# Performance work log

Hardware: AMD Instinct MI355X
Metric: run time of the kernel (lower is better)

Reference implementation:

```python
import jax, jax.numpy as jnp
import numpy as np

D_MODEL, D_STATE, B, S = 1024, 64, 8, 2048


def setup_inputs() -> dict:
    key = jax.random.key(0)
    ks = jax.random.split(key, 14)
    inp = {"x": jax.random.normal(ks[0], (B, S, D_MODEL), jnp.float32)}
    names = ["cog", "beh", "env", "delta", "Bp", "Cp"]
    for i, n in enumerate(names):
        inp[f"W_{n}"] = jax.random.normal(ks[1 + 2 * i], (D_STATE, D_MODEL), jnp.float32) / np.sqrt(D_MODEL)
        inp[f"b_{n}"] = jnp.zeros((D_STATE,), jnp.float32)
    # torch init is log(|randn|+1e-4); we use strictly-negative A_log so the
    # length-2048 multiplicative recurrence stays finite (A_log is a learned
    # parameter, so its value is free; the math of forward is unchanged).
    inp["A_log"] = -jnp.abs(jax.random.normal(ks[13], (D_STATE, D_STATE), jnp.float32)) - 0.1
    return inp


def reference(x, W_cog, b_cog, W_beh, b_beh, W_env, b_env,
              W_delta, b_delta, W_Bp, b_Bp, W_Cp, b_Cp, A_log):
    # gating terms (computed in the source but never used downstream)
    A_t = (jax.nn.sigmoid(x @ W_cog.T + b_cog)
           * jax.nn.sigmoid(x @ W_beh.T + b_beh)
           * jax.nn.sigmoid(x @ W_env.T + b_env))
    del A_t

    delta = jax.nn.softplus(x @ W_delta.T + b_delta)   # [B,S,N]
    Bt = x @ W_Bp.T + b_Bp                             # [B,S,N]
    Ct = x @ W_Cp.T + b_Cp                             # [B,S,N]
    u = Bt * x[:, :, :D_STATE]                         # [B,S,N]

    # Faithful to torch broadcasting: after step 0 the carried state h is
    # [B,N,N] with h[b,i,j] = exp(A_log[i,j]*delta[b,t,i]) * h_prev[b,i,j] + u[b,t,j]
    def step(h, td):
        d, u_t, c_t = td                               # each [B,N]
        A = jnp.exp(A_log[None, :, :] * d[:, :, None]) # [B,N,N]
        h = A * h + u_t[:, None, :]
        y = jnp.einsum('bj,bij->bi', c_t, h)           # [B,N]
        return h, y

    h0 = jnp.zeros((x.shape[0], D_STATE, D_STATE), x.dtype)
    _, ys = jax.lax.scan(
        step, h0,
        (delta.transpose(1, 0, 2), u.transpose(1, 0, 2), Ct.transpose(1, 0, 2)))
    # torch stacks y_t of shape [B,1,N] along dim=1 -> [B,S,1,N]
    return ys.transpose(1, 0, 2)[:, :, None, :]
```

## Files before the change

### kernel.cpp

```cpp
#include <hip/hip_runtime.h>
#include <math.h>

#define DM   1024
#define DS   64
#define BATCH 8
#define SEQ  2048
#define CL   32
#define NC   64

typedef __bf16 bf16x8 __attribute__((ext_vector_type(8)));
typedef __bf16 bf16x4 __attribute__((ext_vector_type(4)));
typedef float  f32x4  __attribute__((ext_vector_type(4)));

__global__ __launch_bounds__(256) void wconv_kernel(
    const float* __restrict__ Wd, const float* __restrict__ Wb,
    const float* __restrict__ Wc, __bf16* __restrict__ Wp)
{
    int idx = blockIdx.x * 256 + threadIdx.x;
    int k  = idx & 1023;
    int n  = idx >> 10;
    const float* W = (n < 64) ? Wd : (n < 128 ? Wb : Wc);
    float v = W[(size_t)(n & 63) * DM + k];
    int kt = k >> 5, kk = k & 31;
    Wp[((size_t)kt * 192 + n) * 32 + kk] = (__bf16)v;
}

__global__ __launch_bounds__(256) void proj_mfma(
    const float* __restrict__ x, const __bf16* __restrict__ Wp,
    const float* __restrict__ bd, const float* __restrict__ bb,
    const float* __restrict__ bc,
    float* __restrict__ delta_g, float* __restrict__ u_g,
    float* __restrict__ ct_g)
{
    __shared__ __bf16 sA[2][32 * 40];
    __shared__ __bf16 sB[2][192 * 40];

    const int tid  = threadIdx.x;
    const int row0 = blockIdx.x * 32;

    const int sx_row = tid >> 3;
    const int sx_sub = tid & 7;
    const float* xg = x + (size_t)(row0 + sx_row) * DM + sx_sub * 4;
    const int wn0  = tid >> 2;
    const int wsub = tid & 3;

    const int lane = tid & 63, wv = tid >> 6;
    const int l15 = lane & 15, quad = lane >> 4;
    const int mrow  = (wv & 1) * 16;
    const int nbase = (wv >> 1) * 96;

    f32x4 acc[6];
    #pragma unroll
    for (int i = 0; i < 6; ++i) acc[i] = (f32x4){0.f, 0.f, 0.f, 0.f};

    float4 xr;
    uint4 w0, w1, w2;

    #define LOAD(kt) do {                                                     \
        xr = *(const float4*)(xg + (kt) * 32);                                \
        const __bf16* wp = Wp + ((size_t)(kt) * 192) * 32 + wsub * 8;         \
        w0 = *(const uint4*)(wp + (size_t)(wn0      ) * 32);                  \
        w1 = *(const uint4*)(wp + (size_t)(wn0 +  64) * 32);                  \
        w2 = *(const uint4*)(wp + (size_t)(wn0 + 128) * 32);                  \
    } while (0)

    #define STAGE(bi) do {                                                    \
        bf16x4 hv = {(__bf16)xr.x, (__bf16)xr.y, (__bf16)xr.z, (__bf16)xr.w}; \
        *(bf16x4*)&sA[bi][sx_row * 40 + sx_sub * 4] = hv;                     \
        *(uint4*)&sB[bi][(wn0      ) * 40 + wsub * 8] = w0;                   \
        *(uint4*)&sB[bi][(wn0 +  64) * 40 + wsub * 8] = w1;                   \
        *(uint4*)&sB[bi][(wn0 + 128) * 40 + wsub * 8] = w2;                   \
    } while (0)

    #define COMPUTE(bi) do {                                                  \
        bf16x8 ah = *(const bf16x8*)&sA[bi][(mrow + l15) * 40 + quad * 8];    \
        _Pragma("unroll")                                                     \
        for (int nt = 0; nt < 6; ++nt) {                                      \
            bf16x8 bf = *(const bf16x8*)                                      \
                &sB[bi][(nbase + nt * 16 + l15) * 40 + quad * 8];             \
            acc[nt] = __builtin_amdgcn_mfma_f32_16x16x32_bf16(                \
                ah, bf, acc[nt], 0, 0, 0);                                    \
        }                                                                     \
    } while (0)

    LOAD(0);
    STAGE(0);
    __syncthreads();

    int buf = 0;
    for (int kt = 0; kt < 32; ++kt) {
        if (kt < 31) LOAD(kt + 1);
        COMPUTE(buf);
        if (kt < 31) STAGE(buf ^ 1);
        __syncthreads();
        buf ^= 1;
    }

    #pragma unroll
    for (int nt = 0; nt < 6; ++nt) {
        int gn  = nbase + nt * 16 + l15;
        int mat = gn >> 6;
        int col = gn & 63;
        float bias = (mat == 0) ? bd[col] : (mat == 1 ? bb[col] : bc[col]);
        #pragma unroll
        for (int r = 0; r < 4; ++r) {
            int m = row0 + mrow + quad * 4 + r;
            float v = acc[nt][r] + bias;
            if (mat == 0) {
                float sp = (v > 20.f) ? v : log1pf(__expf(v));
                delta_g[(size_t)m * DS + col] = sp;
            } else if (mat == 1) {
                u_g[(size_t)m * DS + col] = v * x[(size_t)m * DM + col];
            } else {
                ct_g[(size_t)m * DS + col] = v;
            }
        }
    }
    #undef LOAD
    #undef STAGE
    #undef COMPUTE
}

__global__ __launch_bounds__(256) void pass1_kernel(
    const float* __restrict__ delta_g, const float* __restrict__ u_g,
    const float* __restrict__ A_log,
    float* __restrict__ E, float* __restrict__ Dsum)
{
    __shared__ float s_d[CL * 64];
    __shared__ float s_u[CL * 64];
    const int c = blockIdx.x, b = blockIdx.y, tid = threadIdx.x;
    const int t0 = c * CL;

    const float4* dg = (const float4*)(delta_g + ((size_t)b * SEQ + t0) * DS);
    const float4* ug = (const float4*)(u_g     + ((size_t)b * SEQ + t0) * DS);
    #pragma unroll
    for (int it = 0; it < (CL * 64 / 4) / 256; ++it) {
        int f = tid + it * 256;
        ((float4*)s_d)[f] = dg[f];
        ((float4*)s_u)[f] = ug[f];
    }

    const int i  = tid & 63;
    const int jg = tid >> 6;
    float alog[16];
    {
        const float4* ar = (const float4*)(A_log + i * 64 + jg * 16);
        #pragma unroll
        for (int q = 0; q < 4; ++q) {
            float4 v = ar[q];
            alog[4*q+0] = v.x; alog[4*q+1] = v.y;
            alog[4*q+2] = v.z; alog[4*q+3] = v.w;
        }
    }
    __syncthreads();

    float h[16];
    #pragma unroll
    for (int k = 0; k < 16; ++k) h[k] = 0.f;
    float dsum = 0.f;

    for (int t = 0; t < CL; ++t) {
        float d = s_d[t * 64 + i];
        dsum += d;
        const float* up = s_u + t * 64 + jg * 16;
        #pragma unroll
        for (int k = 0; k < 16; ++k)
            h[k] = __expf(alog[k] * d) * h[k] + up[k];
    }

    float* eo = E + (((size_t)c * BATCH + b) * 64 + i) * 64 + jg * 16;
    #pragma unroll
    for (int q = 0; q < 4; ++q)
        ((float4*)eo)[q] = make_float4(h[4*q], h[4*q+1], h[4*q+2], h[4*q+3]);
    if (jg == 0) Dsum[((size_t)c * BATCH + b) * 64 + i] = dsum;
}

__global__ __launch_bounds__(256) void pass2_kernel(
    const float* __restrict__ A_log, const float* __restrict__ E,
    const float* __restrict__ Dsum, float* __restrict__ Sin)
{
    const int g = blockIdx.x * 256 + threadIdx.x;
    const int b = g >> 12;
    const int e = g & 4095;
    const int i = e >> 6;
    const float al = A_log[e];

    float Eb[4], db[4];
    #pragma unroll
    for (int p = 0; p < 4; ++p) {
        size_t nb = (size_t)p * BATCH + b;
        Eb[p] = E[nb * 4096 + e];
        db[p] = __expf(al * Dsum[nb * 64 + i]);
    }

    float carry = 0.f;
    #pragma unroll 4
    for (int c = 0; c < NC; ++c) {
        const int s = c & 3;
        float Ec = Eb[s], dc = db[s];
        if (c + 4 < NC) {
            size_t nb = (size_t)(c + 4) * BATCH + b;
            Eb[s] = E[nb * 4096 + e];
            db[s] = __expf(al * Dsum[nb * 64 + i]);
        }
        Sin[((size_t)c * BATCH + b) * 4096 + e] = carry;
        carry = dc * carry + Ec;
    }
}

__global__ __launch_bounds__(256) void pass3_kernel(
    const float* __restrict__ delta_g, const float* __restrict__ u_g,
    const float* __restrict__ ct_g, const float* __restrict__ A_log,
    const float* __restrict__ Sin, float* __restrict__ out)
{
    __shared__ float s_d[CL * 64];
    __shared__ float s_u[CL * 64];
    __shared__ float s_c[CL * 64];

    const int c = blockIdx.x, b = blockIdx.y, tid = threadIdx.x;
    const int t0 = c * CL;

    const float4* dg = (const float4*)(delta_g + ((size_t)b * SEQ + t0) * DS);
    const float4* ug = (const float4*)(u_g     + ((size_t)b * SEQ + t0) * DS);
    const float4* cg = (const float4*)(ct_g    + ((size_t)b * SEQ + t0) * DS);
    #pragma unroll
    for (int it = 0; it < (CL * 64 / 4) / 256; ++it) {
        int f = tid + it * 256;
        ((float4*)s_d)[f] = dg[f];
        ((float4*)s_u)[f] = ug[f];
        ((float4*)s_c)[f] = cg[f];
    }

    const int i  = tid >> 2;
    const int jg = tid & 3;

    float alog[16];
    {
        const float4* ar = (const float4*)(A_log + i * 64 + jg * 16);
        #pragma unroll
        for (int q = 0; q < 4; ++q) {
            float4 v = ar[q];
            alog[4*q+0] = v.x; alog[4*q+1] = v.y;
            alog[4*q+2] = v.z; alog[4*q+3] = v.w;
        }
    }

    float h[16];
    {
        const float4* hin = (const float4*)(
            Sin + (((size_t)c * BATCH + b) * 64 + i) * 64 + jg * 16);
        #pragma unroll
        for (int q = 0; q < 4; ++q) {
            float4 v = hin[q];
            h[4*q+0] = v.x; h[4*q+1] = v.y; h[4*q+2] = v.z; h[4*q+3] = v.w;
        }
    }
    __syncthreads();

    for (int t = 0; t < CL; ++t) {
        float d = s_d[t * 64 + i];
        const float* up = s_u + t * 64 + jg * 16;
        const float* cp = s_c + t * 64 + jg * 16;
        float part = 0.f;
        #pragma unroll
        for (int k = 0; k < 16; ++k) {
            h[k] = __expf(alog[k] * d) * h[k] + up[k];
            part += cp[k] * h[k];
        }
        part += __shfl_xor(part, 1);
        part += __shfl_xor(part, 2);
        if (jg == 0)
            out[((size_t)b * SEQ + t0 + t) * DS + i] = part;
    }
}

extern "C" void kernel_launch(void* const* d_in, const int* in_sizes, int n_in,
                              void* d_out, int out_size, void* d_ws, size_t ws_size,
                              hipStream_t stream)
{
    const float* x     = (const float*)d_in[0];
    const float* Wd    = (const float*)d_in[7];
    const float* bd    = (const float*)d_in[8];
    const float* Wb    = (const float*)d_in[9];
    const float* bb    = (const float*)d_in[10];
    const float* Wc    = (const float*)d_in[11];
    const float* bc    = (const float*)d_in[12];
    const float* A_log = (const float*)d_in[13];
    float* out = (float*)d_out;

    float* ws = (float*)d_ws;
    float* delta_g = ws;
    float* u_g     = ws + 1 * 1048576;
    float* ct_g    = ws + 2 * 1048576;
    float* E       = ws + 3 * 1048576;
    float* Sin     = ws + 5 * 1048576;
    float* Dsum    = ws + 7 * 1048576;
    __bf16* Wp     = (__bf16*)E;

    wconv_kernel<<<768, 256, 0, stream>>>(Wd, Wb, Wc, Wp);
    proj_mfma<<<512, 256, 0, stream>>>(
        x, Wp, bd, bb, bc, delta_g, u_g, ct_g);
    pass1_kernel<<<dim3(NC, BATCH), 256, 0, stream>>>(
        delta_g, u_g, A_log, E, Dsum);
    pass2_kernel<<<(BATCH * 4096) / 256, 256, 0, stream>>>(
        A_log, E, Dsum, Sin);
    pass3_kernel<<<dim3(NC, BATCH), 256, 0, stream>>>(
        delta_g, u_g, ct_g, A_log, Sin, out);
}
```

Baseline: 204.2 us.

## Restructure projection GEMM to register-direct split-K and use exp2 in scans

The projection kernel no longer stages x and weights through LDS. Each wave loads its A and B fragments straight from global memory into registers with double buffering, and K is split across wave pairs with an LDS reduction at the end. The scan kernels fold log2(e) into A_log so they can call exp2f directly instead of __expf. pass2 is relaunched with 64-thread blocks to get more blocks. The register-direct loads give up the weight reuse across waves that LDS provided and raise register pressure (24 uint4 buffers).

```diff
diff --git a/kernel.cpp b/kernel.cpp
--- a/kernel.cpp
+++ b/kernel.cpp
@@ -9,7 +9,6 @@
 #define NC   64
 
 typedef __bf16 bf16x8 __attribute__((ext_vector_type(8)));
-typedef __bf16 bf16x4 __attribute__((ext_vector_type(4)));
 typedef float  f32x4  __attribute__((ext_vector_type(4)));
 
 __global__ __launch_bounds__(256) void wconv_kernel(
@@ -32,93 +31,97 @@
     float* __restrict__ delta_g, float* __restrict__ u_g,
     float* __restrict__ ct_g)
 {
-    __shared__ __bf16 sA[2][32 * 40];
-    __shared__ __bf16 sB[2][192 * 40];
+    __shared__ float sAcc[2][64][48];
 
     const int tid  = threadIdx.x;
-    const int row0 = blockIdx.x * 32;
-
-    const int sx_row = tid >> 3;
-    const int sx_sub = tid & 7;
-    const float* xg = x + (size_t)(row0 + sx_row) * DM + sx_sub * 4;
-    const int wn0  = tid >> 2;
-    const int wsub = tid & 3;
-
-    const int lane = tid & 63, wv = tid >> 6;
-    const int l15 = lane & 15, quad = lane >> 4;
-    const int mrow  = (wv & 1) * 16;
-    const int nbase = (wv >> 1) * 96;
-
-    f32x4 acc[6];
-    #pragma unroll
-    for (int i = 0; i < 6; ++i) acc[i] = (f32x4){0.f, 0.f, 0.f, 0.f};
-
-    float4 xr;
-    uint4 w0, w1, w2;
-
-    #define LOAD(kt) do {                                                     \
-        xr = *(const float4*)(xg + (kt) * 32);                                \
-        const __bf16* wp = Wp + ((size_t)(kt) * 192) * 32 + wsub * 8;         \
-        w0 = *(const uint4*)(wp + (size_t)(wn0      ) * 32);                  \
-        w1 = *(const uint4*)(wp + (size_t)(wn0 +  64) * 32);                  \
-        w2 = *(const uint4*)(wp + (size_t)(wn0 + 128) * 32);                  \
+    const int wv   = tid >> 6;
+    const int lane = tid & 63;
+    const int l15  = lane & 15, quad = lane >> 4;
+    const int w_m  = wv & 1;
+    const int w_k  = wv >> 1;
+    const int row0 = blockIdx.x * 32 + w_m * 16;
+
+    const float*  xg = x + (size_t)(row0 + l15) * DM + quad * 8;
+    const __bf16* wg = Wp + (size_t)l15 * 32 + quad * 8;
+
+    f32x4 acc[12];
+    #pragma unroll
+    for (int i = 0; i < 12; ++i) acc[i] = (f32x4){0.f, 0.f, 0.f, 0.f};
+
+    float4 aA0, aA1, aB0, aB1;
+    uint4  bA[12], bB[12];
+
+    #define LOADA(s0, s1, kt) do {                                            \
+        s0 = *(const float4*)(xg + (kt) * 32);                                \
+        s1 = *(const float4*)(xg + (kt) * 32 + 4);                            \
     } while (0)
-
-    #define STAGE(bi) do {                                                    \
-        bf16x4 hv = {(__bf16)xr.x, (__bf16)xr.y, (__bf16)xr.z, (__bf16)xr.w}; \
-        *(bf16x4*)&sA[bi][sx_row * 40 + sx_sub * 4] = hv;                     \
-        *(uint4*)&sB[bi][(wn0      ) * 40 + wsub * 8] = w0;                   \
-        *(uint4*)&sB[bi][(wn0 +  64) * 40 + wsub * 8] = w1;                   \
-        *(uint4*)&sB[bi][(wn0 + 128) * 40 + wsub * 8] = w2;                   \
+    #define LOADB(dst, kt) do {                                               \
+        const __bf16* p = wg + (size_t)(kt) * (192 * 32);                     \
+        _Pragma("unroll")                                                     \
+        for (int nt = 0; nt < 12; ++nt)                                       \
+            dst[nt] = *(const uint4*)(p + (size_t)nt * (16 * 32));            \
     } while (0)
-
-    #define COMPUTE(bi) do {                                                  \
-        bf16x8 ah = *(const bf16x8*)&sA[bi][(mrow + l15) * 40 + quad * 8];    \
+    #define COMPUTE(s0, s1, bsrc) do {                                        \
+        bf16x8 av = {(__bf16)s0.x, (__bf16)s0.y, (__bf16)s0.z, (__bf16)s0.w,  \
+                     (__bf16)s1.x, (__bf16)s1.y, (__bf16)s1.z, (__bf16)s1.w}; \
         _Pragma("unroll")                                                     \
-        for (int nt = 0; nt < 6; ++nt) {                                      \
-            bf16x8 bf = *(const bf16x8*)                                      \
-                &sB[bi][(nbase + nt * 16 + l15) * 40 + quad * 8];             \
+        for (int nt = 0; nt < 12; ++nt)                                       \
             acc[nt] = __builtin_amdgcn_mfma_f32_16x16x32_bf16(                \
-                ah, bf, acc[nt], 0, 0, 0);                                    \
-        }                                                                     \
+                av, __builtin_bit_cast(bf16x8, bsrc[nt]), acc[nt], 0, 0, 0);  \
     } while (0)
 
-    LOAD(0);
-    STAGE(0);
+    const int kt0 = w_k * 16;
+    LOADA(aA0, aA1, kt0);
+    LOADB(bA, kt0);
+
+    #pragma unroll
+    for (int k2 = 0; k2 < 8; ++k2) {
+        const int kt = kt0 + k2 * 2;
+        LOADB(bB, kt + 1);
+        LOADA(aB0, aB1, kt + 1);
+        COMPUTE(aA0, aA1, bA);
+        if (k2 < 7) {
+            LOADA(aA0, aA1, kt + 2);
+            LOADB(bA, kt + 2);
+        }
+        COMPUTE(aB0, aB1, bB);
+    }
+    #undef LOADA
+    #undef LOADB
+    #undef COMPUTE
+
+    if (w_k == 1) {
+        #pragma unroll
+        for (int nt = 0; nt < 12; ++nt)
+            *(f32x4*)&sAcc[w_m][lane][nt * 4] = acc[nt];
+    }
     __syncthreads();
-
-    int buf = 0;
-    for (int kt = 0; kt < 32; ++kt) {
-        if (kt < 31) LOAD(kt + 1);
-        COMPUTE(buf);
-        if (kt < 31) STAGE(buf ^ 1);
-        __syncthreads();
-        buf ^= 1;
-    }
-
-    #pragma unroll
-    for (int nt = 0; nt < 6; ++nt) {
-        int gn  = nbase + nt * 16 + l15;
-        int mat = gn >> 6;
-        int col = gn & 63;
-        float bias = (mat == 0) ? bd[col] : (mat == 1 ? bb[col] : bc[col]);
-        #pragma unroll
-        for (int r = 0; r < 4; ++r) {
-            int m = row0 + mrow + quad * 4 + r;
-            float v = acc[nt][r] + bias;
-            if (mat == 0) {
-                float sp = (v > 20.f) ? v : log1pf(__expf(v));
-                delta_g[(size_t)m * DS + col] = sp;
-            } else if (mat == 1) {
-                u_g[(size_t)m * DS + col] = v * x[(size_t)m * DM + col];
-            } else {
-                ct_g[(size_t)m * DS + col] = v;
+    if (w_k == 0) {
+        #pragma unroll
+        for (int nt = 0; nt < 12; ++nt) {
+            f32x4 o = *(const f32x4*)&sAcc[w_m][lane][nt * 4];
+            acc[nt] += o;
+        }
+        #pragma unroll
+        for (int nt = 0; nt < 12; ++nt) {
+            int mat = nt >> 2;
+            int col = ((nt & 3) << 4) + l15;
+            float bias = (mat == 0) ? bd[col] : (mat == 1 ? bb[col] : bc[col]);
+            #pragma unroll
+            for (int r = 0; r < 4; ++r) {
+                int m = row0 + quad * 4 + r;
+                float v = acc[nt][r] + bias;
+                if (mat == 0) {
+                    float sp = (v > 20.f) ? v : log1pf(__expf(v));
+                    delta_g[(size_t)m * DS + col] = sp;
+                } else if (mat == 1) {
+                    u_g[(size_t)m * DS + col] = v * x[(size_t)m * DM + col];
+                } else {
+                    ct_g[(size_t)m * DS + col] = v;
+                }
             }
         }
     }
-    #undef LOAD
-    #undef STAGE
-    #undef COMPUTE
 }
 
 __global__ __launch_bounds__(256) void pass1_kernel(
@@ -148,8 +151,8 @@
         #pragma unroll
         for (int q = 0; q < 4; ++q) {
             float4 v = ar[q];
-            alog[4*q+0] = v.x; alog[4*q+1] = v.y;
-            alog[4*q+2] = v.z; alog[4*q+3] = v.w;
+            alog[4*q+0] = v.x * 1.44269504f; alog[4*q+1] = v.y * 1.44269504f;
+            alog[4*q+2] = v.z * 1.44269504f; alog[4*q+3] = v.w * 1.44269504f;
         }
     }
     __syncthreads();
@@ -165,7 +168,7 @@
         const float* up = s_u + t * 64 + jg * 16;
         #pragma unroll
         for (int k = 0; k < 16; ++k)
-            h[k] = __expf(alog[k] * d) * h[k] + up[k];
+            h[k] = exp2f(alog[k] * d) * h[k] + up[k];
     }
 
     float* eo = E + (((size_t)c * BATCH + b) * 64 + i) * 64 + jg * 16;
@@ -175,22 +178,22 @@
     if (jg == 0) Dsum[((size_t)c * BATCH + b) * 64 + i] = dsum;
 }
 
-__global__ __launch_bounds__(256) void pass2_kernel(
+__global__ __launch_bounds__(64) void pass2_kernel(
     const float* __restrict__ A_log, const float* __restrict__ E,
     const float* __restrict__ Dsum, float* __restrict__ Sin)
 {
-    const int g = blockIdx.x * 256 + threadIdx.x;
+    const int g = blockIdx.x * 64 + threadIdx.x;
     const int b = g >> 12;
     const int e = g & 4095;
     const int i = e >> 6;
-    const float al = A_log[e];
+    const float al = A_log[e] * 1.44269504f;
 
     float Eb[4], db[4];
     #pragma unroll
     for (int p = 0; p < 4; ++p) {
         size_t nb = (size_t)p * BATCH + b;
         Eb[p] = E[nb * 4096 + e];
-        db[p] = __expf(al * Dsum[nb * 64 + i]);
+        db[p] = exp2f(al * Dsum[nb * 64 + i]);
     }
 
     float carry = 0.f;
@@ -201,7 +204,7 @@
         if (c + 4 < NC) {
             size_t nb = (size_t)(c + 4) * BATCH + b;
             Eb[s] = E[nb * 4096 + e];
-            db[s] = __expf(al * Dsum[nb * 64 + i]);
+            db[s] = exp2f(al * Dsum[nb * 64 + i]);
         }
         Sin[((size_t)c * BATCH + b) * 4096 + e] = carry;
         carry = dc * carry + Ec;
@@ -240,8 +243,8 @@
         #pragma unroll
         for (int q = 0; q < 4; ++q) {
             float4 v = ar[q];
-            alog[4*q+0] = v.x; alog[4*q+1] = v.y;
-            alog[4*q+2] = v.z; alog[4*q+3] = v.w;
+            alog[4*q+0] = v.x * 1.44269504f; alog[4*q+1] = v.y * 1.44269504f;
+            alog[4*q+2] = v.z * 1.44269504f; alog[4*q+3] = v.w * 1.44269504f;
         }
     }
 
@@ -264,7 +267,7 @@
         float part = 0.f;
         #pragma unroll
         for (int k = 0; k < 16; ++k) {
-            h[k] = __expf(alog[k] * d) * h[k] + up[k];
+            h[k] = exp2f(alog[k] * d) * h[k] + up[k];
             part += cp[k] * h[k];
         }
         part += __shfl_xor(part, 1);
@@ -302,7 +305,7 @@
         x, Wp, bd, bb, bc, delta_g, u_g, ct_g);
     pass1_kernel<<<dim3(NC, BATCH), 256, 0, stream>>>(
         delta_g, u_g, A_log, E, Dsum);
-    pass2_kernel<<<(BATCH * 4096) / 256, 256, 0, stream>>>(
+    pass2_kernel<<<512, 64, 0, stream>>>(
         A_log, E, Dsum, Sin);
     pass3_kernel<<<dim3(NC, BATCH), 256, 0, stream>>>(
         delta_g, u_g, ct_g, A_log, Sin, out);
```

After: 219.3 us. 7.4% more time.

## Retile projection GEMM with 32x32 MFMA, use exp2 in scan passes

Applied to the files above, without the earlier changes.

The projection GEMM now uses 64-row blocks with 32x32x16 bf16 MFMA instructions. It loads the x fragments straight from global memory into registers, dropping the A shared-memory staging, and double-buffers two K-tiles of weights per iteration. The scan kernels pre-scale A_log by log2(e) and use the hardware exp2 instruction instead of __expf. Pass2 prefetches eight chunks ahead instead of four. The aim is to cut LDS traffic, instruction count and the latency of exponentials, at the cost of more registers (launch bounds of 1 block) and fewer, larger GEMM blocks.

```diff
diff --git a/kernel.cpp b/kernel.cpp
--- a/kernel.cpp
+++ b/kernel.cpp
@@ -9,8 +9,14 @@
 #define NC   64
 
 typedef __bf16 bf16x8 __attribute__((ext_vector_type(8)));
-typedef __bf16 bf16x4 __attribute__((ext_vector_type(4)));
 typedef float  f32x4  __attribute__((ext_vector_type(4)));
+typedef float  f32x16 __attribute__((ext_vector_type(16)));
+
+#if __has_builtin(__builtin_amdgcn_exp2f)
+#define EXP2(v) __builtin_amdgcn_exp2f(v)
+#else
+#define EXP2(v) __expf(0.69314718056f * (v))
+#endif
 
 __global__ __launch_bounds__(256) void wconv_kernel(
     const float* __restrict__ Wd, const float* __restrict__ Wb,
@@ -25,89 +31,115 @@
     Wp[((size_t)kt * 192 + n) * 32 + kk] = (__bf16)v;
 }
 
-__global__ __launch_bounds__(256) void proj_mfma(
+__global__ __launch_bounds__(256, 1) void proj_mfma(
     const float* __restrict__ x, const __bf16* __restrict__ Wp,
     const float* __restrict__ bd, const float* __restrict__ bb,
     const float* __restrict__ bc,
     float* __restrict__ delta_g, float* __restrict__ u_g,
     float* __restrict__ ct_g)
 {
-    __shared__ __bf16 sA[2][32 * 40];
-    __shared__ __bf16 sB[2][192 * 40];
+    __shared__ __bf16 sB[2][192 * 72];
 
     const int tid  = threadIdx.x;
-    const int row0 = blockIdx.x * 32;
-
-    const int sx_row = tid >> 3;
-    const int sx_sub = tid & 7;
-    const float* xg = x + (size_t)(row0 + sx_row) * DM + sx_sub * 4;
-    const int wn0  = tid >> 2;
-    const int wsub = tid & 3;
+    const int row0 = blockIdx.x * 64;
 
     const int lane = tid & 63, wv = tid >> 6;
-    const int l15 = lane & 15, quad = lane >> 4;
-    const int mrow  = (wv & 1) * 16;
-    const int nbase = (wv >> 1) * 96;
-
-    f32x4 acc[6];
-    #pragma unroll
-    for (int i = 0; i < 6; ++i) acc[i] = (f32x4){0.f, 0.f, 0.f, 0.f};
-
-    float4 xr;
-    uint4 w0, w1, w2;
-
-    #define LOAD(kt) do {                                                     \
-        xr = *(const float4*)(xg + (kt) * 32);                                \
-        const __bf16* wp = Wp + ((size_t)(kt) * 192) * 32 + wsub * 8;         \
-        w0 = *(const uint4*)(wp + (size_t)(wn0      ) * 32);                  \
-        w1 = *(const uint4*)(wp + (size_t)(wn0 +  64) * 32);                  \
-        w2 = *(const uint4*)(wp + (size_t)(wn0 + 128) * 32);                  \
-    } while (0)
-
-    #define STAGE(bi) do {                                                    \
-        bf16x4 hv = {(__bf16)xr.x, (__bf16)xr.y, (__bf16)xr.z, (__bf16)xr.w}; \
-        *(bf16x4*)&sA[bi][sx_row * 40 + sx_sub * 4] = hv;                     \
-        *(uint4*)&sB[bi][(wn0      ) * 40 + wsub * 8] = w0;                   \
-        *(uint4*)&sB[bi][(wn0 +  64) * 40 + wsub * 8] = w1;                   \
-        *(uint4*)&sB[bi][(wn0 + 128) * 40 + wsub * 8] = w2;                   \
-    } while (0)
-
-    #define COMPUTE(bi) do {                                                  \
-        bf16x8 ah = *(const bf16x8*)&sA[bi][(mrow + l15) * 40 + quad * 8];    \
+    const int l31  = lane & 31, q = lane >> 5;
+    const int mbase = row0 + (wv & 1) * 32;
+    const int nhalf = (wv >> 1) * 96;
+
+    const float* xrow = x + (size_t)(mbase + l31) * DM;
+
+    f32x16 acc[3];
+    #pragma unroll
+    for (int i = 0; i < 3; ++i)
+        acc[i] = (f32x16){0,0,0,0,0,0,0,0,0,0,0,0,0,0,0,0};
+
+    float4 aC[8], aN[8];
+    uint4  wreg[6];
+
+    #define LOADB(kb) do {                                                    \
         _Pragma("unroll")                                                     \
-        for (int nt = 0; nt < 6; ++nt) {                                      \
-            bf16x8 bf = *(const bf16x8*)                                      \
-                &sB[bi][(nbase + nt * 16 + l15) * 40 + quad * 8];             \
-            acc[nt] = __builtin_amdgcn_mfma_f32_16x16x32_bf16(                \
-                ah, bf, acc[nt], 0, 0, 0);                                    \
+        for (int it = 0; it < 6; ++it) {                                      \
+            int g   = tid + it * 256;                                         \
+            int ktl = (it >= 3) ? 1 : 0;                                      \
+            int r   = g - ktl * 768;                                          \
+            int n   = r >> 2, c4 = r & 3;                                     \
+            wreg[it] = *(const uint4*)(                                       \
+                Wp + ((size_t)((kb) * 2 + ktl) * 192 + n) * 32 + c4 * 8);     \
         }                                                                     \
     } while (0)
-
-    LOAD(0);
-    STAGE(0);
+    #define STAGEB(bi) do {                                                   \
+        _Pragma("unroll")                                                     \
+        for (int it = 0; it < 6; ++it) {                                      \
+            int g   = tid + it * 256;                                         \
+            int ktl = (it >= 3) ? 1 : 0;                                      \
+            int r   = g - ktl * 768;                                          \
+            int n   = r >> 2, c4 = r & 3;                                     \
+            *(uint4*)&sB[bi][n * 72 + ktl * 32 + c4 * 8] = wreg[it];          \
+        }                                                                     \
+    } while (0)
+    #define LOADA(dst, kb) do {                                               \
+        _Pragma("unroll")                                                     \
+        for (int s = 0; s < 4; ++s) {                                         \
+            dst[2*s]   = *(const float4*)(xrow + (kb)*64 + s*16 + q*8);       \
+            dst[2*s+1] = *(const float4*)(xrow + (kb)*64 + s*16 + q*8 + 4);   \
+        }                                                                     \
+    } while (0)
+    #define COMPUTE(bi) do {                                                  \
+        _Pragma("unroll")                                                     \
+        for (int s = 0; s < 4; ++s) {                                         \
+            float4 a0 = aC[2*s], a1 = aC[2*s+1];                              \
+            bf16x8 av = {(__bf16)a0.x, (__bf16)a0.y, (__bf16)a0.z,            \
+                         (__bf16)a0.w, (__bf16)a1.x, (__bf16)a1.y,            \
+                         (__bf16)a1.z, (__bf16)a1.w};                         \
+            _Pragma("unroll")                                                 \
+            for (int nt = 0; nt < 3; ++nt) {                                  \
+                bf16x8 bv = *(const bf16x8*)                                  \
+                    &sB[bi][(nhalf + nt*32 + l31) * 72 + s*16 + q*8];         \
+                acc[nt] = __builtin_amdgcn_mfma_f32_32x32x16_bf16(            \
+                    av, bv, acc[nt], 0, 0, 0);                                \
+            }                                                                 \
+        }                                                                     \
+    } while (0)
+
+    LOADB(0);
+    STAGEB(0);
+    LOADA(aC, 0);
     __syncthreads();
 
     int buf = 0;
-    for (int kt = 0; kt < 32; ++kt) {
-        if (kt < 31) LOAD(kt + 1);
+    for (int kb = 0; kb < 16; ++kb) {
+        if (kb < 15) {
+            LOADB(kb + 1);
+            LOADA(aN, kb + 1);
+        }
         COMPUTE(buf);
-        if (kt < 31) STAGE(buf ^ 1);
+        if (kb < 15) STAGEB(buf ^ 1);
         __syncthreads();
+        if (kb < 15) {
+            #pragma unroll
+            for (int i = 0; i < 8; ++i) aC[i] = aN[i];
+        }
         buf ^= 1;
     }
-
-    #pragma unroll
-    for (int nt = 0; nt < 6; ++nt) {
-        int gn  = nbase + nt * 16 + l15;
-        int mat = gn >> 6;
+    #undef LOADB
+    #undef STAGEB
+    #undef LOADA
+    #undef COMPUTE
+
+    #pragma unroll
+    for (int nt = 0; nt < 3; ++nt) {
+        int gn  = nhalf + nt * 32 + l31;
+        int mat = (nhalf + nt * 32) >> 6;
         int col = gn & 63;
         float bias = (mat == 0) ? bd[col] : (mat == 1 ? bb[col] : bc[col]);
         #pragma unroll
-        for (int r = 0; r < 4; ++r) {
-            int m = row0 + mrow + quad * 4 + r;
+        for (int r = 0; r < 16; ++r) {
+            int m = mbase + (r & 3) + 8 * (r >> 2) + 4 * q;
             float v = acc[nt][r] + bias;
             if (mat == 0) {
-                float sp = (v > 20.f) ? v : log1pf(__expf(v));
+                float sp = (v > 20.f) ? v : __logf(1.f + __expf(v));
                 delta_g[(size_t)m * DS + col] = sp;
             } else if (mat == 1) {
                 u_g[(size_t)m * DS + col] = v * x[(size_t)m * DM + col];
@@ -116,9 +148,6 @@
             }
         }
     }
-    #undef LOAD
-    #undef STAGE
-    #undef COMPUTE
 }
 
 __global__ __launch_bounds__(256) void pass1_kernel(
@@ -146,10 +175,10 @@
     {
         const float4* ar = (const float4*)(A_log + i * 64 + jg * 16);
         #pragma unroll
-        for (int q = 0; q < 4; ++q) {
-            float4 v = ar[q];
-            alog[4*q+0] = v.x; alog[4*q+1] = v.y;
-            alog[4*q+2] = v.z; alog[4*q+3] = v.w;
+        for (int qq = 0; qq < 4; ++qq) {
+            float4 v = ar[qq];
+            alog[4*qq+0] = v.x * 1.44269504f; alog[4*qq+1] = v.y * 1.44269504f;
+            alog[4*qq+2] = v.z * 1.44269504f; alog[4*qq+3] = v.w * 1.44269504f;
         }
     }
     __syncthreads();
@@ -165,13 +194,13 @@
         const float* up = s_u + t * 64 + jg * 16;
         #pragma unroll
         for (int k = 0; k < 16; ++k)
-            h[k] = __expf(alog[k] * d) * h[k] + up[k];
+            h[k] = EXP2(alog[k] * d) * h[k] + up[k];
     }
 
     float* eo = E + (((size_t)c * BATCH + b) * 64 + i) * 64 + jg * 16;
     #pragma unroll
-    for (int q = 0; q < 4; ++q)
-        ((float4*)eo)[q] = make_float4(h[4*q], h[4*q+1], h[4*q+2], h[4*q+3]);
+    for (int qq = 0; qq < 4; ++qq)
+        ((float4*)eo)[qq] = make_float4(h[4*qq], h[4*qq+1], h[4*qq+2], h[4*qq+3]);
     if (jg == 0) Dsum[((size_t)c * BATCH + b) * 64 + i] = dsum;
 }
 
@@ -183,25 +212,25 @@
     const int b = g >> 12;
     const int e = g & 4095;
     const int i = e >> 6;
-    const float al = A_log[e];
-
-    float Eb[4], db[4];
-    #pragma unroll
-    for (int p = 0; p < 4; ++p) {
+    const float al = A_log[e] * 1.44269504f;
+
+    float Eb[8], db[8];
+    #pragma unroll
+    for (int p = 0; p < 8; ++p) {
         size_t nb = (size_t)p * BATCH + b;
         Eb[p] = E[nb * 4096 + e];
-        db[p] = __expf(al * Dsum[nb * 64 + i]);
+        db[p] = EXP2(al * Dsum[nb * 64 + i]);
     }
 
     float carry = 0.f;
-    #pragma unroll 4
+    #pragma unroll 8
     for (int c = 0; c < NC; ++c) {
-        const int s = c & 3;
+        const int s = c & 7;
         float Ec = Eb[s], dc = db[s];
-        if (c + 4 < NC) {
-            size_t nb = (size_t)(c + 4) * BATCH + b;
+        if (c + 8 < NC) {
+            size_t nb = (size_t)(c + 8) * BATCH + b;
             Eb[s] = E[nb * 4096 + e];
-            db[s] = __expf(al * Dsum[nb * 64 + i]);
+            db[s] = EXP2(al * Dsum[nb * 64 + i]);
         }
         Sin[((size_t)c * BATCH + b) * 4096 + e] = carry;
         carry = dc * carry + Ec;
@@ -238,10 +267,10 @@
     {
         const float4* ar = (const float4*)(A_log + i * 64 + jg * 16);
         #pragma unroll
-        for (int q = 0; q < 4; ++q) {
-            float4 v = ar[q];
-            alog[4*q+0] = v.x; alog[4*q+1] = v.y;
-            alog[4*q+2] = v.z; alog[4*q+3] = v.w;
+        for (int qq = 0; qq < 4; ++qq) {
+            float4 v = ar[qq];
+            alog[4*qq+0] = v.x * 1.44269504f; alog[4*qq+1] = v.y * 1.44269504f;
+            alog[4*qq+2] = v.z * 1.44269504f; alog[4*qq+3] = v.w * 1.44269504f;
         }
     }
 
@@ -250,9 +279,9 @@
         const float4* hin = (const float4*)(
             Sin + (((size_t)c * BATCH + b) * 64 + i) * 64 + jg * 16);
         #pragma unroll
-        for (int q = 0; q < 4; ++q) {
-            float4 v = hin[q];
-            h[4*q+0] = v.x; h[4*q+1] = v.y; h[4*q+2] = v.z; h[4*q+3] = v.w;
+        for (int qq = 0; qq < 4; ++qq) {
+            float4 v = hin[qq];
+            h[4*qq+0] = v.x; h[4*qq+1] = v.y; h[4*qq+2] = v.z; h[4*qq+3] = v.w;
         }
     }
     __syncthreads();
@@ -264,7 +293,7 @@
         float part = 0.f;
         #pragma unroll
         for (int k = 0; k < 16; ++k) {
-            h[k] = __expf(alog[k] * d) * h[k] + up[k];
+            h[k] = EXP2(alog[k] * d) * h[k] + up[k];
             part += cp[k] * h[k];
         }
         part += __shfl_xor(part, 1);
@@ -298,11 +327,11 @@
     __bf16* Wp     = (__bf16*)E;
 
     wconv_kernel<<<768, 256, 0, stream>>>(Wd, Wb, Wc, Wp);
-    proj_mfma<<<512, 256, 0, stream>>>(
+    proj_mfma<<<256, 256, 0, stream>>>(
         x, Wp, bd, bb, bc, delta_g, u_g, ct_g);
     pass1_kernel<<<dim3(NC, BATCH), 256, 0, stream>>>(
         delta_g, u_g, A_log, E, Dsum);
-    pass2_kernel<<<(BATCH * 4096) / 256, 256, 0, stream>>>(
+    pass2_kernel<<<128, 256, 0, stream>>>(
         A_log, E, Dsum, Sin);
     pass3_kernel<<<dim3(NC, BATCH), 256, 0, stream>>>(
         delta_g, u_g, ct_g, A_log, Sin, out);
```

New measurement: 199.5 us. 1.02x faster.
